# Kernel optimization log

Measured on AMD Instinct MI355X. Metric: run time of the kernel, lower is better.

Reference implementation:

```python
import jax, jax.numpy as jnp
import numpy as np

B, N, G = 256, 512, 117  # batch, max_num_cells, n_genes
CH = 25                  # Emphsis conv out channels (hidden_d_1st_conv)


def setup_inputs() -> dict:
    key = jax.random.key(0)
    ks = jax.random.split(key, 11)
    images = jax.random.normal(ks[0], (B, N, 1, 7, 7), dtype=jnp.float32)
    spot_images = jax.random.normal(ks[1], (B, 1, 28, 28), dtype=jnp.float32)
    gene_expression = jax.random.normal(ks[2], (B, G), dtype=jnp.float32)
    # Emphsis: Conv2d(1, 25, k=3, s=1) + ReLU
    W_emph = jax.random.normal(ks[3], (CH, 1, 3, 3), dtype=jnp.float32) * 0.2
    b_emph = jax.random.normal(ks[4], (CH,), dtype=jnp.float32) * 0.1
    # 117 stacked GeneBlock Linear(625, 1) heads -> one (G, 625) matrix
    W_reg = jax.random.normal(ks[5], (G, 625), dtype=jnp.float32) * 0.04
    b_reg = jax.random.normal(ks[6], (G,), dtype=jnp.float32) * 0.1
    # PatchEmbedding: Conv2d(1, 3, k=5, s=5)
    W_patch = jax.random.normal(ks[7], (3, 1, 5, 5), dtype=jnp.float32) * 0.2
    b_patch = jax.random.normal(ks[8], (3,), dtype=jnp.float32) * 0.1
    # global_embedding: Linear(75, 1) + ELU
    W_glob = jax.random.normal(ks[9], (1, 75), dtype=jnp.float32) * 0.1
    b_glob = jax.random.normal(ks[10], (1,), dtype=jnp.float32) * 0.1
    return dict(images=images, spot_images=spot_images, gene_expression=gene_expression,
                W_emph=W_emph, b_emph=b_emph, W_reg=W_reg, b_reg=b_reg,
                W_patch=W_patch, b_patch=b_patch, W_glob=W_glob, b_glob=b_glob)


def reference(images, spot_images, gene_expression, W_emph, b_emph, W_reg, b_reg,
              W_patch, b_patch, W_glob, b_glob):
    Bn, Nc = images.shape[0], images.shape[1]
    # Emphsis conv over all (batch, cell) pairs at once: (B*N, 1, 7, 7) -> (B*N, 25, 5, 5)
    x = images.reshape(Bn * Nc, 1, 7, 7)
    t = jax.lax.conv_general_dilated(x, W_emph, window_strides=(1, 1), padding='VALID',
                                     dimension_numbers=('NCHW', 'OIHW', 'NCHW'))
    t = jax.nn.relu(t + b_emph[None, :, None, None])
    flat = t.reshape(Bn, Nc, CH * 5 * 5)  # (B, N, 625)
    # 117 independent Linear(625,1) heads fused into one matmul -> (B, N, G)
    out = jnp.einsum('bnd,gd->bng', flat, W_reg) + b_reg
    # PatchEmbedding: (B,1,28,28) -> (B,3,5,5) -> tokens (B,25,3) -> flatten (B,75)
    s = jax.lax.conv_general_dilated(spot_images, W_patch, window_strides=(5, 5), padding='VALID',
                                     dimension_numbers=('NCHW', 'OIHW', 'NCHW'))
    s = s + b_patch[None, :, None, None]
    s = s.reshape(Bn, 3, 25).transpose(0, 2, 1).reshape(Bn, 75)
    glob = jax.nn.elu(s @ W_glob.T + b_glob)  # (B, 1)
    # out1 broadcast of global embedding over (cells, genes)
    cell = jax.nn.relu(out + glob[:, :, None])  # (B, N, G)
    # F.linear with ones weight over cell axis == sum over cells
    spot = cell.sum(axis=1)  # (B, G)
    out1 = jnp.broadcast_to(glob[:, :, None], (Bn, Nc, out.shape[2]))  # (B, N, G)
    return spot, cell, out1
```

## Files before the change

### kernel.cpp

```cpp
#include <hip/hip_runtime.h>


typedef __attribute__((ext_vector_type(16))) float f32x16;
typedef __attribute__((ext_vector_type(8))) short short8;
typedef __attribute__((ext_vector_type(2))) unsigned int uint2v;
typedef __attribute__((ext_vector_type(4))) unsigned int uint4v;

#define WCOMB_OFF 0
#define GLOB_OFF  245760

#define SPOT_OUT_OFF 0
#define CELL_OUT_OFF 29952
#define OUT1_OUT_OFF 15365376

__device__ __forceinline__ unsigned short f2bf(float x) {
  unsigned int u = __builtin_bit_cast(unsigned int, x);
  u = (u + 0x7FFFu + ((u >> 16) & 1u)) >> 16;
  return (unsigned short)u;
}

__device__ __forceinline__ unsigned int cvt_pk_bf16(float lo, float hi) {
  unsigned int w;
  asm("v_cvt_pk_bf16_f32 %0, %1, %2" : "=v"(w) : "v"(lo), "v"(hi));
  return w;
}

__device__ __forceinline__ void gload16(const void* g, void* l) {
  __builtin_amdgcn_global_load_lds(
      (const __attribute__((address_space(1))) void*)g,
      (__attribute__((address_space(3))) void*)l, 16, 0, 0);
}

__global__ __launch_bounds__(128) void prep_kernel(
    const float* __restrict__ spot_images, const float* __restrict__ W_patch,
    const float* __restrict__ b_patch, const float* __restrict__ W_glob,
    const float* __restrict__ b_glob, const float* __restrict__ W_reg,
    const float* __restrict__ W_emph, const float* __restrict__ b_emph,
    unsigned short* __restrict__ wcomb, float* __restrict__ glob) {
  int bid = blockIdx.x;
  int tid = threadIdx.x;
  if (bid < 256) {
    __shared__ float red[75];
    if (tid < 75) {
      int token = tid / 3;
      int chan = tid - token * 3;
      int ty = token / 5, tx = token - ty * 5;
      const float* img = spot_images + bid * 784 + (ty * 5) * 28 + tx * 5;
      float a = 0.f;
      #pragma unroll
      for (int i = 0; i < 5; ++i)
        #pragma unroll
        for (int j = 0; j < 5; ++j)
          a = fmaf(img[i * 28 + j], W_patch[chan * 25 + i * 5 + j], a);
      a += b_patch[chan];
      red[tid] = a * W_glob[tid];
    }
    __syncthreads();
    if (tid == 0) {
      float s = b_glob[0];
      for (int k = 0; k < 75; ++k) s += red[k];
      glob[bid] = (s > 0.f) ? s : expm1f(s);
    }
  } else if (bid < 336) {
    int idx = bid - 256;
    int jt = idx >> 2, s = idx & 3;
    if (tid < 64) {
      int j = jt * 32 + (tid & 31);
      int h = tid >> 5;
      unsigned short hv[8];
      #pragma unroll
      for (int jj = 0; jj < 8; ++jj) {
        int i = s * 16 + h * 8 + jj;
        float val = 0.f;
        if (j < 625) {
          int ch = j / 25, p = j % 25;
          int oy = p / 5, ox = p - oy * 5;
          if (i < 49) {
            int iy = i / 7, ix = i - iy * 7;
            int ky = iy - oy, kx = ix - ox;
            if (ky >= 0 && ky < 3 && kx >= 0 && kx < 3)
              val = W_emph[ch * 9 + ky * 3 + kx];
          } else if (i == 49) {
            val = b_emph[ch];
          }
        }
        hv[jj] = f2bf(val);
      }
      unsigned int u[4];
      #pragma unroll
      for (int k = 0; k < 4; ++k)
        u[k] = (unsigned int)hv[2 * k] | ((unsigned int)hv[2 * k + 1] << 16);
      ((uint4*)wcomb)[jt * 768 + s * 64 + tid] = make_uint4(u[0], u[1], u[2], u[3]);
    }
  } else {
    int idx = bid - 336;
    int sg = idx >> 2, q = idx & 3;
    if (tid < 64) {
      int g = q * 32 + (tid & 31);
      int h = tid >> 5;
      unsigned short hv[8];
      #pragma unroll
      for (int jj = 0; jj < 8; ++jj) {
        int k = sg * 16 + h * 8 + jj;
        float val = (g < 117 && k < 625) ? W_reg[g * 625 + k] : 0.f;
        hv[jj] = f2bf(val);
      }
      unsigned int u[4];
      #pragma unroll
      for (int k = 0; k < 4; ++k)
        u[k] = (unsigned int)hv[2 * k] | ((unsigned int)hv[2 * k + 1] << 16);
      int jt = sg >> 1, c = (sg & 1) * 4 + q;
      ((uint4*)wcomb)[jt * 768 + 256 + c * 64 + tid] =
          make_uint4(u[0], u[1], u[2], u[3]);
    }
  }
}

__global__ __launch_bounds__(512, 2) void main_kernel(
    const float* __restrict__ images, const float* __restrict__ b_reg,
    const unsigned short* __restrict__ wcomb, const float* __restrict__ glob,
    float* __restrict__ out) {
  __shared__ char smem[59392];
  unsigned short* imgbs = (unsigned short*)smem;
  char* wbuf = smem + 32768;
  float* C = (float*)smem;
  float* red = (float*)(smem + 57344);
  int tid = threadIdx.x;
  int b = blockIdx.x;
  int l = tid & 63;
  int ct = __builtin_amdgcn_readfirstlane(tid >> 6);
  int m = l & 31, hh = l >> 5;
  const char* wcombB = (const char*)wcomb;
  const short8* imgb8 = (const short8*)imgbs;

  float gb = glob[b];
  size_t rowbase = (size_t)b * 512;
  float4 gv = make_float4(gb, gb, gb, gb);
  float4* o1v = (float4*)(out + OUT1_OUT_OFF + rowbase * 117);

  auto stage = [&](int jt, int buf) {
    const char* s0 = wcombB + jt * 12288 + ct * 1024 + l * 16;
    char* d0 = wbuf + buf * 12288 + ct * 1024;
    gload16(s0, d0);
    if (ct < 4) gload16(s0 + 8192, d0 + 8192);
  };

  auto stageimg = [&](int hf) {
    #pragma unroll
    for (int it = 0; it < 4; ++it) {
      int u = it * 512 + tid;
      int cell = u & 255, kc = u >> 8;
      const float* src =
          images + (size_t)(b * 512 + hf * 256 + cell) * 49 + kc * 8;
      float v[8];
      #pragma unroll
      for (int j = 0; j < 8; ++j) v[j] = 0.f;
      if (kc < 6) {
        #pragma unroll
        for (int j = 0; j < 8; ++j) v[j] = src[j];
      } else if (kc == 6) {
        v[0] = src[0];
        v[1] = 1.0f;
      }
      unsigned int uu[4];
      #pragma unroll
      for (int k = 0; k < 4; ++k) uu[k] = cvt_pk_bf16(v[2 * k], v[2 * k + 1]);
      ((uint4*)imgbs)[kc * 256 + cell] = make_uint4(uu[0], uu[1], uu[2], uu[3]);
    }
  };

  short8 bU0, bU1, bU2, bU3, bV0, bV1, bV2, bV3;
  int base = (ct & 3) * 64;
  stageimg(0);
  __syncthreads();
  if (ct < 4) {
    bU0 = imgb8[(0 + hh) * 256 + base + m];
    bU1 = imgb8[(2 + hh) * 256 + base + m];
    bU2 = imgb8[(4 + hh) * 256 + base + m];
    bU3 = imgb8[(6 + hh) * 256 + base + m];
    bV0 = imgb8[(0 + hh) * 256 + base + 32 + m];
    bV1 = imgb8[(2 + hh) * 256 + base + 32 + m];
    bV2 = imgb8[(4 + hh) * 256 + base + 32 + m];
    bV3 = imgb8[(6 + hh) * 256 + base + 32 + m];
  }
  __syncthreads();
  stageimg(1);
  __syncthreads();
  if (ct >= 4) {
    bU0 = imgb8[(0 + hh) * 256 + base + m];
    bU1 = imgb8[(2 + hh) * 256 + base + m];
    bU2 = imgb8[(4 + hh) * 256 + base + m];
    bU3 = imgb8[(6 + hh) * 256 + base + m];
    bV0 = imgb8[(0 + hh) * 256 + base + 32 + m];
    bV1 = imgb8[(2 + hh) * 256 + base + 32 + m];
    bV2 = imgb8[(4 + hh) * 256 + base + 32 + m];
    bV3 = imgb8[(6 + hh) * 256 + base + 32 + m];
  }
  stage(0, 0);
  __syncthreads();

  f32x16 aU0, aU1, aU2, aU3, aV0, aV1, aV2, aV3;
  #pragma unroll
  for (int i = 0; i < 16; ++i) {
    aU0[i] = 0.f; aU1[i] = 0.f; aU2[i] = 0.f; aU3[i] = 0.f;
    aV0[i] = 0.f; aV1[i] = 0.f; aV2[i] = 0.f; aV3[i] = 0.f;
  }

  for (int jt = 0; jt < 20; ++jt) {
    if (jt < 19) stage(jt + 1, (jt + 1) & 1);
    if (jt < 15) {
      int i0 = jt * 1024 + tid;
      o1v[i0] = gv;
      int i1 = i0 + 512;
      if (i1 < 14976) o1v[i1] = gv;
    }

    const short8* wB = (const short8*)(wbuf + (jt & 1) * 12288);
    short8 a0 = wB[l];
    short8 a1 = wB[64 + l];
    short8 a2 = wB[128 + l];
    short8 a3 = wB[192 + l];

    f32x16 o;
    #pragma unroll
    for (int i = 0; i < 16; ++i) o[i] = 0.f;
    o = __builtin_amdgcn_mfma_f32_32x32x16_bf16(a0, bU0, o, 0, 0, 0);
    o = __builtin_amdgcn_mfma_f32_32x32x16_bf16(a1, bU1, o, 0, 0, 0);
    o = __builtin_amdgcn_mfma_f32_32x32x16_bf16(a2, bU2, o, 0, 0, 0);
    o = __builtin_amdgcn_mfma_f32_32x32x16_bf16(a3, bU3, o, 0, 0, 0);
    unsigned int W[8];
    #pragma unroll
    for (int q = 0; q < 8; ++q)
      W[q] = cvt_pk_bf16(fmaxf(o[2 * q], 0.f), fmaxf(o[2 * q + 1], 0.f));
    uint2v s02 = __builtin_amdgcn_permlane32_swap(W[0], W[2], false, false);
    uint2v s13 = __builtin_amdgcn_permlane32_swap(W[1], W[3], false, false);
    uint2v s46 = __builtin_amdgcn_permlane32_swap(W[4], W[6], false, false);
    uint2v s57 = __builtin_amdgcn_permlane32_swap(W[5], W[7], false, false);
    uint4v f0 = {s02[0], s13[0], s02[1], s13[1]};
    uint4v f1 = {s46[0], s57[0], s46[1], s57[1]};
    short8 afU0 = __builtin_bit_cast(short8, f0);
    short8 afU1 = __builtin_bit_cast(short8, f1);

    #pragma unroll
    for (int i = 0; i < 16; ++i) o[i] = 0.f;
    o = __builtin_amdgcn_mfma_f32_32x32x16_bf16(a0, bV0, o, 0, 0, 0);
    o = __builtin_amdgcn_mfma_f32_32x32x16_bf16(a1, bV1, o, 0, 0, 0);
    o = __builtin_amdgcn_mfma_f32_32x32x16_bf16(a2, bV2, o, 0, 0, 0);
    o = __builtin_amdgcn_mfma_f32_32x32x16_bf16(a3, bV3, o, 0, 0, 0);
    #pragma unroll
    for (int q = 0; q < 8; ++q)
      W[q] = cvt_pk_bf16(fmaxf(o[2 * q], 0.f), fmaxf(o[2 * q + 1], 0.f));
    s02 = __builtin_amdgcn_permlane32_swap(W[0], W[2], false, false);
    s13 = __builtin_amdgcn_permlane32_swap(W[1], W[3], false, false);
    s46 = __builtin_amdgcn_permlane32_swap(W[4], W[6], false, false);
    s57 = __builtin_amdgcn_permlane32_swap(W[5], W[7], false, false);
    uint4v g0 = {s02[0], s13[0], s02[1], s13[1]};
    uint4v g1 = {s46[0], s57[0], s46[1], s57[1]};
    short8 afV0 = __builtin_bit_cast(short8, g0);
    short8 afV1 = __builtin_bit_cast(short8, g1);

    #define MM2(c, AFU, AFV, AU, AV)                                        \
      {                                                                     \
        short8 w = wB[256 + (c)*64 + l];                                    \
        AU = __builtin_amdgcn_mfma_f32_32x32x16_bf16(AFU, w, AU, 0, 0, 0);  \
        AV = __builtin_amdgcn_mfma_f32_32x32x16_bf16(AFV, w, AV, 0, 0, 0);  \
      }
    MM2(0, afU0, afV0, aU0, aV0)
    MM2(1, afU0, afV0, aU1, aV1)
    MM2(2, afU0, afV0, aU2, aV2)
    MM2(3, afU0, afV0, aU3, aV3)
    MM2(4, afU1, afV1, aU0, aV0)
    MM2(5, afU1, afV1, aU1, aV1)
    MM2(6, afU1, afV1, aU2, aV2)
    MM2(7, afU1, afV1, aU3, aV3)
    #undef MM2

    __syncthreads();
  }

  float br0 = (0 * 32 + m < 117) ? b_reg[0 * 32 + m] : 0.f;
  float br1 = (1 * 32 + m < 117) ? b_reg[1 * 32 + m] : 0.f;
  float br2 = (2 * 32 + m < 117) ? b_reg[2 * 32 + m] : 0.f;
  float br3 = (3 * 32 + m < 117) ? b_reg[3 * 32 + m] : 0.f;

  float part = 0.f;
  for (int p = 0; p < 8; ++p) {
    if (ct == p) {
      #define EPI(Q, ACC, NB, BR)                                          \
        {                                                                  \
          int g = (Q)*32 + m;                                              \
          _Pragma("unroll")                                                \
          for (int reg = 0; reg < 16; ++reg) {                             \
            int n = (NB) + (reg & 3) + 8 * (reg >> 2) + 4 * hh;            \
            C[n * 128 + g] = fmaxf(ACC[reg] + (BR) + gb, 0.f);             \
          }                                                                \
        }
      EPI(0, aU0, 0, br0) EPI(1, aU1, 0, br1)
      EPI(2, aU2, 0, br2) EPI(3, aU3, 0, br3)
      EPI(0, aV0, 32, br0) EPI(1, aV1, 32, br1)
      EPI(2, aV2, 32, br2) EPI(3, aV3, 32, br3)
      #undef EPI
    }
    __syncthreads();
    float cellreg[15];
    #pragma unroll
    for (int i = 0; i < 15; ++i) {
      int idx = i * 512 + tid;
      int n = idx / 117;
      int gg = idx - n * 117;
      cellreg[i] = (idx < 7488) ? C[n * 128 + gg] : 0.f;
    }
    {
      int grp = tid >> 7, t = tid & 127;
      float s = 0.f;
      #pragma unroll
      for (int n = 0; n < 16; ++n) s += C[(grp * 16 + n) * 128 + t];
      red[grp * 128 + t] = s;
    }
    __syncthreads();
    if (tid < 128)
      part += red[tid] + red[128 + tid] + red[256 + tid] + red[384 + tid];
    float* cellchunk = out + CELL_OUT_OFF + (rowbase + p * 64) * 117;
    #pragma unroll
    for (int i = 0; i < 15; ++i) {
      int idx = i * 512 + tid;
      if (idx < 7488) cellchunk[idx] = cellreg[i];
    }
  }
  if (tid < 117) out[SPOT_OUT_OFF + b * 117 + tid] = part;
}

extern "C" void kernel_launch(void* const* d_in, const int* in_sizes, int n_in,
                              void* d_out, int out_size, void* d_ws, size_t ws_size,
                              hipStream_t stream) {
  const float* images      = (const float*)d_in[0];
  const float* spot_images = (const float*)d_in[1];
  const float* W_emph = (const float*)d_in[3];
  const float* b_emph = (const float*)d_in[4];
  const float* W_reg  = (const float*)d_in[5];
  const float* b_reg  = (const float*)d_in[6];
  const float* W_patch = (const float*)d_in[7];
  const float* b_patch = (const float*)d_in[8];
  const float* W_glob  = (const float*)d_in[9];
  const float* b_glob  = (const float*)d_in[10];
  float* out = (float*)d_out;

  unsigned short* wcomb = (unsigned short*)((char*)d_ws + WCOMB_OFF);
  float* glob  = (float*)((char*)d_ws + GLOB_OFF);

  prep_kernel<<<496, 128, 0, stream>>>(spot_images, W_patch, b_patch, W_glob,
                                       b_glob, W_reg, W_emph, b_emph, wcomb,
                                       glob);
  main_kernel<<<256, 512, 0, stream>>>(images, b_reg, wcomb, glob, out);
}
```

Before: 51.27 us.

## Stage weights in two large LDS halves and double-buffer cell epilogue

Replaces the per-iteration double-buffered weight staging and its 20 block barriers with two bulk loads of ten weight tiles each into a large LDS slab, leaving only a few barriers in the main loop. The spot reduction is now computed directly from the accumulator registers with a cross-half shuffle, so the C-tile summation pass goes away. The cell epilogue writes 128-row chunks into two alternating LDS buffers, so filling one buffer overlaps with streaming the other to global memory. The price is about 152KB of dynamic shared memory, which permits only one block per CU instead of two, and the second weight half is loaded with no overlap.

```diff
diff --git a/kernel.cpp b/kernel.cpp
--- a/kernel.cpp
+++ b/kernel.cpp
@@ -12,6 +12,8 @@
 #define SPOT_OUT_OFF 0
 #define CELL_OUT_OFF 29952
 #define OUT1_OUT_OFF 15365376
+
+#define SMEM_BYTES 155648
 
 __device__ __forceinline__ unsigned short f2bf(float x) {
   unsigned int u = __builtin_bit_cast(unsigned int, x);
@@ -120,11 +122,12 @@
     const float* __restrict__ images, const float* __restrict__ b_reg,
     const unsigned short* __restrict__ wcomb, const float* __restrict__ glob,
     float* __restrict__ out) {
-  __shared__ char smem[59392];
+  extern __shared__ char smem[];
   unsigned short* imgbs = (unsigned short*)smem;
-  char* wbuf = smem + 32768;
-  float* C = (float*)smem;
-  float* red = (float*)(smem + 57344);
+  char* wslab = smem + 32768;
+  float* C0 = (float*)smem;
+  float* C1 = (float*)(smem + 65536);
+  float* redp = (float*)(smem + 131072);
   int tid = threadIdx.x;
   int b = blockIdx.x;
   int l = tid & 63;
@@ -138,11 +141,12 @@
   float4 gv = make_float4(gb, gb, gb, gb);
   float4* o1v = (float4*)(out + OUT1_OUT_OFF + rowbase * 117);
 
-  auto stage = [&](int jt, int buf) {
-    const char* s0 = wcombB + jt * 12288 + ct * 1024 + l * 16;
-    char* d0 = wbuf + buf * 12288 + ct * 1024;
-    gload16(s0, d0);
-    if (ct < 4) gload16(s0 + 8192, d0 + 8192);
+  auto stage_half = [&](int h) {
+    #pragma unroll
+    for (int i = 0; i < 15; ++i) {
+      int c = ct + 8 * i;
+      gload16(wcombB + h * 122880 + c * 1024 + l * 16, wslab + c * 1024);
+    }
   };
 
   auto stageimg = [&](int hf) {
@@ -196,7 +200,7 @@
     bV2 = imgb8[(4 + hh) * 256 + base + 32 + m];
     bV3 = imgb8[(6 + hh) * 256 + base + 32 + m];
   }
-  stage(0, 0);
+  stage_half(0);
   __syncthreads();
 
   f32x16 aU0, aU1, aU2, aU3, aV0, aV1, aV2, aV3;
@@ -206,16 +210,14 @@
     aV0[i] = 0.f; aV1[i] = 0.f; aV2[i] = 0.f; aV3[i] = 0.f;
   }
 
-  for (int jt = 0; jt < 20; ++jt) {
-    if (jt < 19) stage(jt + 1, (jt + 1) & 1);
+  auto body = [&](int jl, int jt) {
     if (jt < 15) {
       int i0 = jt * 1024 + tid;
       o1v[i0] = gv;
       int i1 = i0 + 512;
       if (i1 < 14976) o1v[i1] = gv;
     }
-
-    const short8* wB = (const short8*)(wbuf + (jt & 1) * 12288);
+    const short8* wB = (const short8*)(wslab + jl * 12288);
     short8 a0 = wB[l];
     short8 a1 = wB[64 + l];
     short8 a2 = wB[128 + l];
@@ -274,60 +276,91 @@
     MM2(6, afU1, afV1, aU2, aV2)
     MM2(7, afU1, afV1, aU3, aV3)
     #undef MM2
-
-    __syncthreads();
-  }
+  };
+
+  for (int jl = 0; jl < 10; ++jl) body(jl, jl);
+  __syncthreads();
+  stage_half(1);
+  __syncthreads();
+  for (int jl = 0; jl < 10; ++jl) body(jl, 10 + jl);
+  __syncthreads();
 
   float br0 = (0 * 32 + m < 117) ? b_reg[0 * 32 + m] : 0.f;
   float br1 = (1 * 32 + m < 117) ? b_reg[1 * 32 + m] : 0.f;
   float br2 = (2 * 32 + m < 117) ? b_reg[2 * 32 + m] : 0.f;
   float br3 = (3 * 32 + m < 117) ? b_reg[3 * 32 + m] : 0.f;
 
-  float part = 0.f;
-  for (int p = 0; p < 8; ++p) {
-    if (ct == p) {
-      #define EPI(Q, ACC, NB, BR)                                          \
-        {                                                                  \
-          int g = (Q)*32 + m;                                              \
-          _Pragma("unroll")                                                \
-          for (int reg = 0; reg < 16; ++reg) {                             \
-            int n = (NB) + (reg & 3) + 8 * (reg >> 2) + 4 * hh;            \
-            C[n * 128 + g] = fmaxf(ACC[reg] + (BR) + gb, 0.f);             \
-          }                                                                \
-        }
-      EPI(0, aU0, 0, br0) EPI(1, aU1, 0, br1)
-      EPI(2, aU2, 0, br2) EPI(3, aU3, 0, br3)
-      EPI(0, aV0, 32, br0) EPI(1, aV1, 32, br1)
-      EPI(2, aV2, 32, br2) EPI(3, aV3, 32, br3)
-      #undef EPI
-    }
-    __syncthreads();
-    float cellreg[15];
-    #pragma unroll
-    for (int i = 0; i < 15; ++i) {
+  {
+    auto rsum = [&](const f32x16& AU, const f32x16& AV, float br) {
+      float s = 0.f;
+      #pragma unroll
+      for (int reg = 0; reg < 16; ++reg)
+        s += fmaxf(AU[reg] + br + gb, 0.f) + fmaxf(AV[reg] + br + gb, 0.f);
+      s += __shfl_xor(s, 32, 64);
+      return s;
+    };
+    float s0 = rsum(aU0, aV0, br0);
+    float s1 = rsum(aU1, aV1, br1);
+    float s2 = rsum(aU2, aV2, br2);
+    float s3 = rsum(aU3, aV3, br3);
+    if (hh == 0) {
+      redp[ct * 128 + m] = s0;
+      redp[ct * 128 + 32 + m] = s1;
+      redp[ct * 128 + 64 + m] = s2;
+      redp[ct * 128 + 96 + m] = s3;
+    }
+  }
+
+  #define EPI(Cb, Q, ACC, NB, BR)                                          \
+    {                                                                      \
+      int g = (Q)*32 + m;                                                  \
+      _Pragma("unroll")                                                    \
+      for (int reg = 0; reg < 16; ++reg) {                                 \
+        int n = (NB) + (reg & 3) + 8 * (reg >> 2) + 4 * hh;                \
+        (Cb)[n * 128 + g] = fmaxf(ACC[reg] + (BR) + gb, 0.f);              \
+      }                                                                    \
+    }
+  #define EPIW(Cb, e)                                                      \
+    {                                                                      \
+      int nb = (e)*64;                                                     \
+      EPI(Cb, 0, aU0, nb, br0) EPI(Cb, 1, aU1, nb, br1)                    \
+      EPI(Cb, 2, aU2, nb, br2) EPI(Cb, 3, aU3, nb, br3)                    \
+      EPI(Cb, 0, aV0, nb + 32, br0) EPI(Cb, 1, aV1, nb + 32, br1)          \
+      EPI(Cb, 2, aV2, nb + 32, br2) EPI(Cb, 3, aV3, nb + 32, br3)          \
+    }
+  auto streamC = [&](const float* Cb, int r) {
+    float* cellchunk = out + CELL_OUT_OFF + (rowbase + r * 128) * 117;
+    #pragma unroll
+    for (int i = 0; i < 30; ++i) {
       int idx = i * 512 + tid;
-      int n = idx / 117;
-      int gg = idx - n * 117;
-      cellreg[i] = (idx < 7488) ? C[n * 128 + gg] : 0.f;
-    }
-    {
-      int grp = tid >> 7, t = tid & 127;
-      float s = 0.f;
-      #pragma unroll
-      for (int n = 0; n < 16; ++n) s += C[(grp * 16 + n) * 128 + t];
-      red[grp * 128 + t] = s;
-    }
-    __syncthreads();
-    if (tid < 128)
-      part += red[tid] + red[128 + tid] + red[256 + tid] + red[384 + tid];
-    float* cellchunk = out + CELL_OUT_OFF + (rowbase + p * 64) * 117;
-    #pragma unroll
-    for (int i = 0; i < 15; ++i) {
-      int idx = i * 512 + tid;
-      if (idx < 7488) cellchunk[idx] = cellreg[i];
-    }
-  }
-  if (tid < 117) out[SPOT_OUT_OFF + b * 117 + tid] = part;
+      if (idx < 14976) {
+        int n = idx / 117;
+        int gg = idx - n * 117;
+        cellchunk[idx] = Cb[n * 128 + gg];
+      }
+    }
+  };
+
+  if (ct < 2) EPIW(C0, ct & 1);
+  __syncthreads();
+  if (tid < 117) {
+    float s = 0.f;
+    #pragma unroll
+    for (int w = 0; w < 8; ++w) s += redp[w * 128 + tid];
+    out[SPOT_OUT_OFF + b * 117 + tid] = s;
+  }
+  if (ct == 2 || ct == 3) EPIW(C1, ct & 1);
+  streamC(C0, 0);
+  __syncthreads();
+  if (ct == 4 || ct == 5) EPIW(C0, ct & 1);
+  streamC(C1, 1);
+  __syncthreads();
+  if (ct == 6 || ct == 7) EPIW(C1, ct & 1);
+  streamC(C0, 2);
+  __syncthreads();
+  streamC(C1, 3);
+  #undef EPIW
+  #undef EPI
 }
 
 extern "C" void kernel_launch(void* const* d_in, const int* in_sizes, int n_in,
@@ -348,8 +381,13 @@
   unsigned short* wcomb = (unsigned short*)((char*)d_ws + WCOMB_OFF);
   float* glob  = (float*)((char*)d_ws + GLOB_OFF);
 
+  (void)hipFuncSetAttribute((const void*)main_kernel,
+                            hipFuncAttributeMaxDynamicSharedMemorySize,
+                            SMEM_BYTES);
+
   prep_kernel<<<496, 128, 0, stream>>>(spot_images, W_patch, b_patch, W_glob,
                                        b_glob, W_reg, W_emph, b_emph, wcomb,
                                        glob);
-  main_kernel<<<256, 512, 0, stream>>>(images, b_reg, wcomb, glob, out);
-}
+  main_kernel<<<256, 512, SMEM_BYTES, stream>>>(images, b_reg, wcomb, glob,
+                                                out);
+}
```

Measured after the change: 51.17 us. No clear change (-0.2%).
